# Kernel tuning notes

Hardware: AMD Instinct MI355X
Metric: run time of the kernel (lower is better)

Reference implementation:

```python
import jax, jax.numpy as jnp
import numpy as np

N, E, D_NODE, D_EDGE, F = 20000, 320000, 256, 128, 128


def _seg_mean(m, dst, w, n):
    # mean aggregation of edge messages into destination nodes
    s = jax.ops.segment_sum(m, dst, num_segments=n)
    c = jax.ops.segment_sum(w, dst, num_segments=n)
    return s / jnp.maximum(c, 1.0)[:, None]


def _edge_conv(x, e, src, dst, W, b, n, emask=None):
    # EdgeConvRot: per-edge MLP on [x_src, x_dst, edge_attr], mean-scatter to nodes
    m = jnp.concatenate([x[src], x[dst], e], axis=1) @ W + b
    if emask is not None:
        m = m * emask[:, None]
        w = emask
    else:
        w = jnp.ones((m.shape[0],), m.dtype)
    return _seg_mean(m, dst, w, n), m


def setup_inputs() -> dict:
    key = jax.random.key(0)
    ks = iter(jax.random.split(key, 40))

    def p(shape):
        return jax.random.normal(next(ks), shape, jnp.float32) / np.float32(np.sqrt(shape[0]))

    inp = {
        'node_feat': jax.random.normal(next(ks), (N, D_NODE), jnp.float32),
        'edge_feat': jax.random.normal(next(ks), (E, D_EDGE), jnp.float32),
        'edge_index': jax.random.randint(next(ks), (2, E), 0, N),
        'W_red': p((D_NODE, F)), 'b_red': jnp.zeros((F,), jnp.float32),
        'W1': p((2 * F + D_EDGE, F)), 'b1': jnp.zeros((F,), jnp.float32),
        'W2': p((3 * F, F)), 'b2': jnp.zeros((F,), jnp.float32),
        'W3': p((6 * F, F)), 'b3': jnp.zeros((F,), jnp.float32),
        'Wpre': p((3 * F, 2 * F)), 'bpre': jnp.zeros((2 * F,), jnp.float32),
        'Wsub': p((6 * F, F)), 'bsub': jnp.zeros((F,), jnp.float32),
        'W4': p((5 * F, F)), 'b4': jnp.zeros((F,), jnp.float32),
        'Wg': p((2 * F, 1)), 'a_s': p((1,)), 'a_d': p((1,)),
        'Wl1': p((F, 1)), 'bl1': jnp.zeros((1,), jnp.float32),
        'Ww': p((F, 1)), 'bw': jnp.zeros((1,), jnp.float32),
    }
    return inp


def reference(node_feat, edge_feat, edge_index, W_red, b_red, W1, b1, W2, b2,
              W3, b3, Wpre, bpre, Wsub, bsub, W4, b4, Wg, a_s, a_d,
              Wl1, bl1, Ww, bw):
    src, dst = edge_index[0], edge_index[1]
    n = node_feat.shape[0]

    x0 = node_feat @ W_red + b_red
    x1, e1 = _edge_conv(x0, edge_feat, src, dst, W1, b1, n)
    x1, e1 = jax.nn.relu(x1), jax.nn.relu(e1)
    x2, e2 = _edge_conv(x1, e1, src, dst, W2, b2, n)
    x2, e2 = jax.nn.relu(x2), jax.nn.relu(e2)
    # conv3 applied twice with SHARED weights (as in the original)
    x3, e3 = _edge_conv(jnp.concatenate([x2, x1], 1), jnp.concatenate([e2, e1], 1), src, dst, W3, b3, n)
    x3, e3 = jax.nn.relu(x3), jax.nn.relu(e3)
    x3, e3 = _edge_conv(jnp.concatenate([x3, x2], 1), jnp.concatenate([e3, e2], 1), src, dst, W3, b3, n)
    x3, e3 = jax.nn.relu(x3), jax.nn.relu(e3)

    xs1, es1 = _edge_conv(x3, e3, src, dst, Wpre, bpre, n)
    xs1, es1 = jax.nn.relu(xs1), jax.nn.relu(es1)

    # ---- SAGPooling (ratio=0.5) with single-head GATConv scorer (+self-loops) ----
    h = (xs1 @ Wg)[:, 0]                              # [N]
    loop = jnp.arange(n)
    si = jnp.concatenate([src, loop])
    di = jnp.concatenate([dst, loop])
    ea = jax.nn.leaky_relu(h[si] * a_s[0] + h[di] * a_d[0], 0.2)
    emax = jax.ops.segment_max(ea, di, num_segments=n)
    ez = jnp.exp(ea - emax[di])
    denom = jax.ops.segment_sum(ez, di, num_segments=n)
    score = jax.ops.segment_sum((ez / denom[di]) * h[si], di, num_segments=n)

    k = n // 2
    topv, perm = jax.lax.top_k(score, k)
    xp = xs1[perm] * jnp.tanh(topv)[:, None]          # [k, 2F]
    new_idx = jnp.full((n,), -1, jnp.int32).at[perm].set(jnp.arange(k, dtype=jnp.int32))
    keep = (new_idx[src] >= 0) & (new_idx[dst] >= 0)  # static-shape edge mask (filter_adj)
    sp = jnp.where(keep, new_idx[src], 0)
    dp = jnp.where(keep, new_idx[dst], 0)
    emk = keep.astype(xp.dtype)

    xs2, _ = _edge_conv(xp, es1, sp, dp, Wsub, bsub, k, emask=emk)
    xs2 = jax.nn.relu(xs2)

    # scatter merge: x3_2[perm] = x3[perm] + xs2 (perm indices are unique)
    x3_2 = x3.at[perm].add(xs2)

    x4, e4 = _edge_conv(jnp.concatenate([x3_2, x3], 1), e3, src, dst, W4, b4, n)
    x4, e4 = jax.nn.relu(x4), jax.nn.relu(e4)

    x = jax.nn.sigmoid(x4 @ Wl1 + bl1)                # [N, 1]
    w = jax.nn.sigmoid(e4 @ Ww + bw)                  # [E, 1]
    return x, w
```

## Files before the change

kernel.cpp:

```cpp
#include <hip/hip_runtime.h>
#include <cstdint>
#include <cstddef>

#define N_NODES 20000
#define N_EDGES 320000
#define EKCAP   (N_EDGES / 2)

__device__ __forceinline__ float frelu(float x){ return x > 0.f ? x : 0.f; }
__device__ __forceinline__ float fleaky(float x){ return x > 0.f ? x : 0.2f*x; }

__device__ __forceinline__ float wsum(float v){
  #pragma unroll
  for (int o = 32; o > 0; o >>= 1) v += __shfl_down(v, o);
  return v;
}
__device__ __forceinline__ float wmaxr(float v){
  #pragma unroll
  for (int o = 32; o > 0; o >>= 1) v = fmaxf(v, __shfl_down(v, o));
  return v;
}
__device__ __forceinline__ int wsumi(int v){
  #pragma unroll
  for (int o = 32; o > 0; o >>= 1) v += __shfl_down(v, o);
  return v;
}
__device__ __forceinline__ float4 fma4(float s, float4 b, float4 c){
  c.x = fmaf(s, b.x, c.x); c.y = fmaf(s, b.y, c.y);
  c.z = fmaf(s, b.z, c.z); c.w = fmaf(s, b.w, c.w); return c;
}

__global__ __launch_bounds__(256) void sgemm_k(
    const float* __restrict__ A1, int K1, const float* __restrict__ B1,
    const float* __restrict__ bias, float* __restrict__ C, int M, int Nn)
{
  __shared__ float As[16][68];
  __shared__ float Bs[16][64];
  const int t = threadIdx.x;
  const int m0 = blockIdx.y * 64, n0 = blockIdx.x * 64;
  const int tx = t & 15, ty = t >> 4;
  float acc[4][4] = {{0.f}};
  for (int kt = 0; kt < K1; kt += 16) {
    {
      const int row = t >> 2, k4 = (t & 3) * 4;
      const int gm = m0 + row;
      float4 v = make_float4(0.f, 0.f, 0.f, 0.f);
      if (gm < M) v = *(const float4*)(A1 + (size_t)gm * K1 + kt + k4);
      As[k4 + 0][row] = v.x; As[k4 + 1][row] = v.y;
      As[k4 + 2][row] = v.z; As[k4 + 3][row] = v.w;
      const int r = t >> 4, c4 = (t & 15) * 4;
      *(float4*)&Bs[r][c4] = *(const float4*)(B1 + (size_t)(kt + r) * Nn + n0 + c4);
    }
    __syncthreads();
    #pragma unroll
    for (int kk = 0; kk < 16; ++kk) {
      const float4 a = *(const float4*)&As[kk][ty * 4];
      const float4 b = *(const float4*)&Bs[kk][tx * 4];
      acc[0][0] += a.x * b.x; acc[0][1] += a.x * b.y; acc[0][2] += a.x * b.z; acc[0][3] += a.x * b.w;
      acc[1][0] += a.y * b.x; acc[1][1] += a.y * b.y; acc[1][2] += a.y * b.z; acc[1][3] += a.y * b.w;
      acc[2][0] += a.z * b.x; acc[2][1] += a.z * b.y; acc[2][2] += a.z * b.z; acc[2][3] += a.z * b.w;
      acc[3][0] += a.w * b.x; acc[3][1] += a.w * b.y; acc[3][2] += a.w * b.z; acc[3][3] += a.w * b.w;
    }
    __syncthreads();
  }
  float4 bv = make_float4(0.f, 0.f, 0.f, 0.f);
  if (bias) bv = *(const float4*)(bias + n0 + tx * 4);
  #pragma unroll
  for (int i = 0; i < 4; ++i) {
    const int gm = m0 + ty * 4 + i;
    if (gm >= M) continue;
    float4 o;
    o.x = acc[i][0] + bv.x; o.y = acc[i][1] + bv.y;
    o.z = acc[i][2] + bv.z; o.w = acc[i][3] + bv.w;
    *(float4*)(C + (size_t)gm * Nn + n0 + tx * 4) = o;
  }
}

__global__ __launch_bounds__(256) void sgemm2_k(
    const float* __restrict__ A1, int K1,
    const float* __restrict__ B1a, const float* __restrict__ B1b,
    const float* __restrict__ A2, int K2,
    const float* __restrict__ B2a, const float* __restrict__ B2b,
    const float* __restrict__ bias,
    float* __restrict__ Ca, float* __restrict__ Cb, int M, int Nn)
{
  __shared__ float As[16][68];
  __shared__ float Bs[16][64];
  const int z = blockIdx.z;
  const float* B1 = z ? B1b : B1a;
  const float* B2 = z ? B2b : B2a;
  float* C = z ? Cb : Ca;
  const float* bs = z ? nullptr : bias;
  const int t = threadIdx.x;
  const int m0 = blockIdx.y * 64, n0 = blockIdx.x * 64;
  const int tx = t & 15, ty = t >> 4;
  float acc[4][4] = {{0.f}};
  for (int pass = 0; pass < 2; ++pass) {
    const float* A = pass ? A2 : A1;
    const float* B = pass ? B2 : B1;
    const int K = pass ? K2 : K1;
    if (A == nullptr) continue;
    for (int kt = 0; kt < K; kt += 16) {
      {
        const int row = t >> 2, k4 = (t & 3) * 4;
        const int gm = m0 + row;
        float4 v = make_float4(0.f, 0.f, 0.f, 0.f);
        if (gm < M) v = *(const float4*)(A + (size_t)gm * K + kt + k4);
        As[k4 + 0][row] = v.x; As[k4 + 1][row] = v.y;
        As[k4 + 2][row] = v.z; As[k4 + 3][row] = v.w;
        const int r = t >> 4, c4 = (t & 15) * 4;
        *(float4*)&Bs[r][c4] = *(const float4*)(B + (size_t)(kt + r) * Nn + n0 + c4);
      }
      __syncthreads();
      #pragma unroll
      for (int kk = 0; kk < 16; ++kk) {
        const float4 a = *(const float4*)&As[kk][ty * 4];
        const float4 b = *(const float4*)&Bs[kk][tx * 4];
        acc[0][0] += a.x * b.x; acc[0][1] += a.x * b.y; acc[0][2] += a.x * b.z; acc[0][3] += a.x * b.w;
        acc[1][0] += a.y * b.x; acc[1][1] += a.y * b.y; acc[1][2] += a.y * b.z; acc[1][3] += a.y * b.w;
        acc[2][0] += a.z * b.x; acc[2][1] += a.z * b.y; acc[2][2] += a.z * b.z; acc[2][3] += a.z * b.w;
        acc[3][0] += a.w * b.x; acc[3][1] += a.w * b.y; acc[3][2] += a.w * b.z; acc[3][3] += a.w * b.w;
      }
      __syncthreads();
    }
  }
  float4 bv = make_float4(0.f, 0.f, 0.f, 0.f);
  if (bs) bv = *(const float4*)(bs + n0 + tx * 4);
  #pragma unroll
  for (int i = 0; i < 4; ++i) {
    const int gm = m0 + ty * 4 + i;
    if (gm >= M) continue;
    float4 o;
    o.x = acc[i][0] + bv.x; o.y = acc[i][1] + bv.y;
    o.z = acc[i][2] + bv.z; o.w = acc[i][3] + bv.w;
    *(float4*)(C + (size_t)gm * Nn + n0 + tx * 4) = o;
  }
}

#define FMA16(J) \
    acc[J][0] = fmaf(a.w, w3.x, fmaf(a.z, w2.x, fmaf(a.y, w1.x, fmaf(a.x, w0.x, acc[J][0])))); \
    acc[J][1] = fmaf(a.w, w3.y, fmaf(a.z, w2.y, fmaf(a.y, w1.y, fmaf(a.x, w0.y, acc[J][1])))); \
    acc[J][2] = fmaf(a.w, w3.z, fmaf(a.z, w2.z, fmaf(a.y, w1.z, fmaf(a.x, w0.z, acc[J][2])))); \
    acc[J][3] = fmaf(a.w, w3.w, fmaf(a.z, w2.w, fmaf(a.y, w1.w, fmaf(a.x, w0.w, acc[J][3]))));

template<int BE, int NOUT, int ASTRIDE, bool RELUIN, bool GATHER, bool STOREM, bool WHEAD, bool SUB>
__global__ __launch_bounds__(256, 4) void econv_k(
    const float* __restrict__ ein0, const float* __restrict__ ein1,
    const float* __restrict__ We,
    const float* __restrict__ P, const float* __restrict__ Q,
    const int* __restrict__ ssrc, const int* __restrict__ sdst,
    const int* __restrict__ seid, const int* __restrict__ nKp,
    float* __restrict__ mout, float* __restrict__ xsum,
    const float* __restrict__ wvec, const float* __restrict__ wb,
    float* __restrict__ outw)
{
  constexpr int NC4 = NOUT / 4;
  constexpr int TE  = 256 / NC4;
  constexpr int EPT = BE / TE;
  __shared__ float smem[8192];
  __shared__ int darr[BE], slotOf[BE], firstE[BE];
  __shared__ int dcount_s, prevd_s, nextd_s;
  const int t = threadIdx.x;
  const int base = blockIdx.x * BE;
  int nvalid = BE;
  int Elim = N_EDGES;
  if constexpr (SUB) {
    const int nK = min(*nKp, EKCAP);
    if (base >= nK) return;
    nvalid = min(BE, nK - base);
    Elim = nK;
  }
  if (t < 64) {
    if (t < BE) {
      int idx = base + t;
      if (SUB && idx >= Elim) idx = Elim - 1;
      darr[t] = sdst[idx];
    }
    if (t == 0) {
      prevd_s = (base > 0) ? sdst[base - 1] : -1;
      nextd_s = (base + BE < Elim) ? sdst[base + BE] : -1;
    }
    const int lane = t;
    const int myd = darr[(lane < BE) ? lane : (BE - 1)];
    int flag = 0;
    if (lane < BE) flag = (lane == 0) || (myd != darr[lane - 1]);
    int s = flag;
    #pragma unroll
    for (int o = 1; o < 64; o <<= 1) {
      const int v = __shfl_up(s, o);
      if (lane >= o) s += v;
    }
    if (lane < BE) {
      slotOf[lane] = s - 1;
      if (flag) firstE[s - 1] = lane;
    }
    if (lane == BE - 1) dcount_s = s;
  }
  const int tx = t % NC4, te = t / NC4;
  const int e0 = te * EPT;
  float4 acc[EPT];
  #pragma unroll
  for (int j = 0; j < EPT; ++j) acc[j] = make_float4(0.f, 0.f, 0.f, 0.f);
  const int nbuf = (ein1 != nullptr) ? 2 : 1;
  for (int buf = 0; buf < nbuf; ++buf) {
    const float* ein = buf ? ein1 : ein0;
    __syncthreads();
    #pragma unroll
    for (int i = t; i < BE * 32; i += 256) {
      const int e = i >> 5, k4 = (i & 31) * 4;
      const int g = base + e;
      const size_t row = GATHER ? (size_t)seid[g] : (size_t)g;
      float4 v = *(const float4*)(ein + row * ASTRIDE + k4);
      if (RELUIN) { v.x = frelu(v.x); v.y = frelu(v.y); v.z = frelu(v.z); v.w = frelu(v.w); }
      *(float4*)&smem[e * 128 + k4] = v;
    }
    __syncthreads();
    const float* Wb = We + (size_t)buf * 128 * NOUT + tx * 4;
    float4 wc0 = *(const float4*)(Wb + 0 * NOUT);
    float4 wc1 = *(const float4*)(Wb + 1 * NOUT);
    float4 wc2 = *(const float4*)(Wb + 2 * NOUT);
    float4 wc3 = *(const float4*)(Wb + 3 * NOUT);
    for (int kg = 0; kg < 32; ++kg) {
      const int kn = (kg < 31) ? (kg + 1) : 31;
      const float* Wn = Wb + (size_t)kn * 4 * NOUT;
      const float4 wn0 = *(const float4*)(Wn);
      const float4 wn1 = *(const float4*)(Wn + NOUT);
      const float4 wn2 = *(const float4*)(Wn + 2 * NOUT);
      const float4 wn3 = *(const float4*)(Wn + 3 * NOUT);
      #pragma unroll
      for (int j = 0; j < EPT; ++j) {
        const float4 a = *(const float4*)&smem[(e0 + j) * 128 + kg * 4];
        acc[j] = fma4(a.x, wc0, acc[j]);
        acc[j] = fma4(a.y, wc1, acc[j]);
        acc[j] = fma4(a.z, wc2, acc[j]);
        acc[j] = fma4(a.w, wc3, acc[j]);
      }
      wc0 = wn0; wc1 = wn1; wc2 = wn2; wc3 = wn3;
    }
  }
  __syncthreads();
  {
    const float4 z = make_float4(0.f, 0.f, 0.f, 0.f);
    for (int i = t * 4; i < BE * NOUT; i += 1024) *(float4*)&smem[i] = z;
  }
  __syncthreads();
  {
    float4 wv = make_float4(0.f, 0.f, 0.f, 0.f);
    if constexpr (WHEAD) wv = *(const float4*)(wvec + tx * 4);
    int cur = darr[e0];
    int slotCur = slotOf[e0];
    float4 q = *(const float4*)(Q + (size_t)cur * NOUT + tx * 4);
    float4 r = make_float4(0.f, 0.f, 0.f, 0.f);
    #pragma unroll
    for (int j = 0; j < EPT; ++j) {
      const int le = e0 + j;
      const int d = darr[le];
      if (d != cur) {
        float* a = &smem[slotCur * NOUT + tx * 4];
        atomicAdd(a + 0, r.x); atomicAdd(a + 1, r.y);
        atomicAdd(a + 2, r.z); atomicAdd(a + 3, r.w);
        cur = d; slotCur = slotOf[le];
        q = *(const float4*)(Q + (size_t)d * NOUT + tx * 4);
        r = make_float4(0.f, 0.f, 0.f, 0.f);
      }
      if (!SUB || le < nvalid) {
        const int g = base + le;
        const int s = ssrc[g];
        const float4 p = *(const float4*)(P + (size_t)s * NOUT + tx * 4);
        float4 m;
        m.x = acc[j].x + p.x + q.x; m.y = acc[j].y + p.y + q.y;
        m.z = acc[j].z + p.z + q.z; m.w = acc[j].w + p.w + q.w;
        if constexpr (STOREM) {
          *(float4*)(mout + (size_t)g * 128 + tx * 4) = m;
        }
        if constexpr (WHEAD) {
          float wp = frelu(m.x) * wv.x + frelu(m.y) * wv.y + frelu(m.z) * wv.z + frelu(m.w) * wv.w;
          #pragma unroll
          for (int o = 16; o > 0; o >>= 1) wp += __shfl_down(wp, o);
          if (tx == 0) outw[seid[g]] = 1.f / (1.f + expf(-(wp + wb[0])));
        }
        r.x += m.x; r.y += m.y; r.z += m.z; r.w += m.w;
      }
    }
    float* a = &smem[slotCur * NOUT + tx * 4];
    atomicAdd(a + 0, r.x); atomicAdd(a + 1, r.y);
    atomicAdd(a + 2, r.z); atomicAdd(a + 3, r.w);
  }
  __syncthreads();
  {
    const int dc = dcount_s;
    const int pd = prevd_s, nd = nextd_s;
    for (int i = t * 4; i < dc * NOUT; i += 1024) {
      const int sidx = i / NOUT, col = i - sidx * NOUT;
      const int d = darr[firstE[sidx]];
      const bool strad = (sidx == 0 && d == pd) || (sidx == dc - 1 && d == nd);
      const float4 v = *(const float4*)&smem[i];
      float* o = xsum + (size_t)d * NOUT + col;
      if (!strad) {
        *(float4*)o = v;
      } else {
        atomicAdd(o + 0, v.x); atomicAdd(o + 1, v.y);
        atomicAdd(o + 2, v.z); atomicAdd(o + 3, v.w);
      }
    }
  }
}

__global__ __launch_bounds__(256, 4) void presub_k(
    const float* __restrict__ e3buf, const float* __restrict__ We,
    const float* __restrict__ P, const float* __restrict__ Q,
    const int* __restrict__ csrc, const int* __restrict__ cdst,
    const int* __restrict__ cidx, const int* __restrict__ nKp,
    float* __restrict__ es1out)
{
  constexpr int BE = 32;
  const int nK = min(*nKp, EKCAP);
  const int base = blockIdx.x * BE;
  if (base >= nK) return;
  __shared__ float As[BE * 128];
  __shared__ float Ws[16 * 256];
  const int t = threadIdx.x;
  const int tx = t & 63, te = t >> 6;
  const int e0 = te * 8;
  float acc[8][4];
  #pragma unroll
  for (int j = 0; j < 8; ++j) { acc[j][0] = 0.f; acc[j][1] = 0.f; acc[j][2] = 0.f; acc[j][3] = 0.f; }
  #pragma unroll
  for (int i = t; i < BE * 32; i += 256) {
    const int e = i >> 5, k4 = (i & 31) * 4;
    const int g = base + e;
    const size_t row = (g < nK) ? (size_t)cidx[g] : 0;
    float4 v = *(const float4*)(e3buf + row * 128 + k4);
    v.x = frelu(v.x); v.y = frelu(v.y); v.z = frelu(v.z); v.w = frelu(v.w);
    *(float4*)&As[e * 128 + k4] = v;
  }
  for (int chunk = 0; chunk < 8; ++chunk) {
    __syncthreads();
    #pragma unroll
    for (int i = t; i < 16 * 64; i += 256) {
      const int r = i >> 6, c4 = (i & 63) * 4;
      *(float4*)&Ws[r * 256 + c4] = *(const float4*)(We + (size_t)(chunk * 16 + r) * 256 + c4);
    }
    __syncthreads();
    #pragma unroll
    for (int kk = 0; kk < 16; kk += 4) {
      const float4 w0 = *(const float4*)&Ws[(kk + 0) * 256 + tx * 4];
      const float4 w1 = *(const float4*)&Ws[(kk + 1) * 256 + tx * 4];
      const float4 w2 = *(const float4*)&Ws[(kk + 2) * 256 + tx * 4];
      const float4 w3 = *(const float4*)&Ws[(kk + 3) * 256 + tx * 4];
      #pragma unroll
      for (int j = 0; j < 8; ++j) {
        const float4 a = *(const float4*)&As[(e0 + j) * 128 + chunk * 16 + kk];
        FMA16(j)
      }
    }
  }
  #pragma unroll
  for (int j = 0; j < 8; ++j) {
    const int g = base + e0 + j;
    if (g < nK) {
      const int s = csrc[g], d = cdst[g];
      const float4 p = *(const float4*)(P + (size_t)s * 256 + tx * 4);
      const float4 q = *(const float4*)(Q + (size_t)d * 256 + tx * 4);
      float4 o;
      o.x = frelu(acc[j][0] + p.x + q.x); o.y = frelu(acc[j][1] + p.y + q.y);
      o.z = frelu(acc[j][2] + p.z + q.z); o.w = frelu(acc[j][3] + p.w + q.w);
      *(float4*)(es1out + (size_t)g * 256 + tx * 4) = o;
    }
  }
}

__global__ void hist_k(const int* __restrict__ dst, int* __restrict__ deg, int E){
  const int e = blockIdx.x * 256 + threadIdx.x;
  if (e < E) atomicAdd(&deg[dst[e]], 1);
}

__global__ __launch_bounds__(1024) void scan_deg_k(
    const int* __restrict__ deg, int* __restrict__ rowstart, int* __restrict__ cursor,
    float* __restrict__ recip, int n)
{
  __shared__ int sb[1024];
  __shared__ int carry;
  const int t = threadIdx.x;
  if (t == 0) carry = 0;
  __syncthreads();
  const int CH = (n + 1023) >> 10;
  for (int c = 0; c < CH; ++c) {
    const int i = c * 1024 + t;
    const int d = (i < n) ? deg[i] : 0;
    sb[t] = d;
    __syncthreads();
    for (int off = 1; off < 1024; off <<= 1) {
      const int v = (t >= off) ? sb[t - off] : 0;
      __syncthreads();
      sb[t] += v;
      __syncthreads();
    }
    const int excl = sb[t] - d;
    const int tot = sb[1023];
    if (i < n) {
      const int rs = carry + excl;
      rowstart[i] = rs; cursor[i] = rs;
      recip[i] = 1.0f / (float)max(d, 1);
    }
    __syncthreads();
    if (t == 0) carry += tot;
    __syncthreads();
  }
  if (t == 0) rowstart[n] = carry;
}

__global__ void scatter_k(const int* __restrict__ src, const int* __restrict__ dst,
                          int* __restrict__ cursor, int* __restrict__ ssrc,
                          int* __restrict__ sdst, int* __restrict__ seid, int E){
  const int e = blockIdx.x * 256 + threadIdx.x;
  if (e < E) {
    const int d = dst[e];
    const int pos = atomicAdd(&cursor[d], 1);
    ssrc[pos] = src[e]; sdst[pos] = d; seid[pos] = e;
  }
}

__global__ void meanrelu_k(const float* __restrict__ xsum, const float* __restrict__ recip,
                           float* __restrict__ out, int total, int shift){
  const int i = blockIdx.x * 256 + threadIdx.x;
  if (i < total) out[i] = frelu(xsum[i] * recip[i >> shift]);
}

__global__ void h_k(const float* __restrict__ xs1, const float* __restrict__ Wg,
                    float* __restrict__ h, int n){
  const int node = blockIdx.x * 4 + (threadIdx.x >> 6);
  const int lane = threadIdx.x & 63;
  if (node >= n) return;
  const float4 x = *(const float4*)(xs1 + (size_t)node * 256 + lane * 4);
  const float4 w = *(const float4*)(Wg + lane * 4);
  float v = x.x * w.x + x.y * w.y + x.z * w.z + x.w * w.w;
  v = wsum(v);
  if (lane == 0) h[node] = v;
}

__global__ void att_k(const float* __restrict__ h, const int* __restrict__ rowstart,
                      const int* __restrict__ ssrc, const float* __restrict__ asp,
                      const float* __restrict__ adp, float* __restrict__ score, int n){
  const int node = blockIdx.x * 4 + (threadIdx.x >> 6);
  const int lane = threadIdx.x & 63;
  if (node >= n) return;
  const float a_s = asp[0], a_d = adp[0];
  const float hv = h[node];
  const int s0 = rowstart[node], s1 = rowstart[node + 1];
  const float selfea = fleaky(hv * (a_s + a_d));
// ... 165 lines not shown
                           const int* __restrict__ cntk, const int* __restrict__ kept,
                           float* __restrict__ x32, int total){
  const int i = blockIdx.x * 256 + threadIdx.x;
  if (i >= total) return;
  const int v = i >> 7;
  float add = 0.f;
  if (kept[v]) {
    float c = (float)cntk[v];
    c = c > 0.f ? c : 1.f;
    add = frelu(xsum[i] / c);
  }
  x32[i] = x3[i] + add;
}

__global__ void fnode_k(const float* __restrict__ xsum, const float* __restrict__ recip,
                        const float* __restrict__ Wl1, const float* __restrict__ bl1,
                        float* __restrict__ out, int n){
  const int node = blockIdx.x * 4 + (threadIdx.x >> 6);
  const int lane = threadIdx.x & 63;
  if (node >= n) return;
  const float rc = recip[node];
  const float2 xv = *(const float2*)(xsum + (size_t)node * 128 + lane * 2);
  const float2 wv = *(const float2*)(Wl1 + lane * 2);
  float v = frelu(xv.x * rc) * wv.x + frelu(xv.y * rc) * wv.y;
  v = wsum(v);
  if (lane == 0) out[node] = 1.f / (1.f + expf(-(v + bl1[0])));
}

extern "C" void kernel_launch(void* const* d_in, const int* in_sizes, int n_in,
                              void* d_out, int out_size, void* d_ws, size_t ws_size,
                              hipStream_t stream)
{
  const int N = N_NODES, E = N_EDGES;
  const float* node_feat = (const float*)d_in[0];
  const float* edge_feat = (const float*)d_in[1];
  const int*   eidx      = (const int*)d_in[2];
  const float* W_red = (const float*)d_in[3];  const float* b_red = (const float*)d_in[4];
  const float* W1 = (const float*)d_in[5];   const float* b1 = (const float*)d_in[6];
  const float* W2 = (const float*)d_in[7];   const float* b2 = (const float*)d_in[8];
  const float* W3 = (const float*)d_in[9];   const float* b3 = (const float*)d_in[10];
  const float* Wpre = (const float*)d_in[11]; const float* bpre = (const float*)d_in[12];
  const float* Wsub = (const float*)d_in[13]; const float* bsub = (const float*)d_in[14];
  const float* W4 = (const float*)d_in[15];  const float* b4 = (const float*)d_in[16];
  const float* Wg = (const float*)d_in[17];
  const float* a_s = (const float*)d_in[18]; const float* a_d = (const float*)d_in[19];
  const float* Wl1 = (const float*)d_in[20]; const float* bl1 = (const float*)d_in[21];
  const float* Ww = (const float*)d_in[22];  const float* bw = (const float*)d_in[23];
  float* out_x = (float*)d_out;
  float* out_w = out_x + N;

  char* wsb = (char*)d_ws;
  size_t off = 0;
  auto alloc = [&](size_t bytes) -> void* {
    void* p = wsb + off;
    off = (off + bytes + 255) & ~(size_t)255;
    return p;
  };
  float* u1   = (float*)alloc((size_t)E * 128 * 4);
  float* u2   = (float*)alloc((size_t)E * 128 * 4);
  float* n1   = (float*)alloc((size_t)N * 128 * 4);
  float* n2   = (float*)alloc((size_t)N * 128 * 4);
  float* n3   = (float*)alloc((size_t)N * 128 * 4);
  float* xs1  = (float*)alloc((size_t)N * 256 * 4);
  float* P    = (float*)alloc((size_t)N * 256 * 4);
  float* Qb   = (float*)alloc((size_t)N * 256 * 4);
  float* xsum = (float*)alloc((size_t)N * 256 * 4);
  int* ssrc = (int*)alloc((size_t)E * 4);
  int* sdst = (int*)alloc((size_t)E * 4);
  int* seid = (int*)alloc((size_t)E * 4);
  int* csrc = (int*)alloc((size_t)E * 4);
  int* cdst = (int*)alloc((size_t)E * 4);
  int* cidx = (int*)alloc((size_t)E * 4);
  int* deg     = (int*)alloc((size_t)N * 4);
  int* cursor  = (int*)alloc((size_t)N * 4);
  int* rowstart= (int*)alloc((size_t)(N + 1) * 4);
  int* kept    = (int*)alloc((size_t)N * 4);
  int* cntk    = (int*)alloc((size_t)N * 4);
  float* recip = (float*)alloc((size_t)N * 4);
  float* hbuf  = (float*)alloc((size_t)N * 4);
  float* score = (float*)alloc((size_t)N * 4);
  float* tfac  = (float*)alloc((size_t)N * 4);
  int* bsum    = (int*)alloc(1024 * 4);
  int* Ek      = (int*)alloc(256);
  (void)ws_size; (void)in_sizes; (void)n_in; (void)out_size;

  const dim3 g128z(2, (N + 63) / 64, 2), g256z(4, (N + 63) / 64, 2);
  const dim3 g128(2, (N + 63) / 64);
  const int nbFS = (E + 1023) / 1024;
  #define NILS nullptr, nullptr, nullptr

  hipMemsetAsync(deg, 0, (size_t)N * 4, stream);
  hist_k<<<(E + 255) / 256, 256, 0, stream>>>(eidx + E, deg, E);
  scan_deg_k<<<1, 1024, 0, stream>>>(deg, rowstart, cursor, recip, N);
  scatter_k<<<(E + 255) / 256, 256, 0, stream>>>(eidx, eidx + E, cursor, ssrc, sdst, seid, E);

  sgemm_k<<<g128, 256, 0, stream>>>(node_feat, 256, W_red, b_red, n1, N, 128);

  sgemm2_k<<<g128z, 256, 0, stream>>>(n1, 128, W1, W1 + 128 * 128,
                                      nullptr, 0, nullptr, nullptr, b1, P, Qb, N, 128);
  hipMemsetAsync(xsum, 0, (size_t)N * 128 * 4, stream);
  econv_k<64, 128, 128, false, true, true, false, false><<<E / 64, 256, 0, stream>>>(
      edge_feat, nullptr, W1 + 256 * 128, P, Qb, ssrc, sdst, seid, nullptr, u1, xsum, NILS);
  meanrelu_k<<<(N * 128) / 256, 256, 0, stream>>>(xsum, recip, n2, N * 128, 7);

  sgemm2_k<<<g128z, 256, 0, stream>>>(n2, 128, W2, W2 + 128 * 128,
                                      nullptr, 0, nullptr, nullptr, b2, P, Qb, N, 128);
  hipMemsetAsync(xsum, 0, (size_t)N * 128 * 4, stream);
  econv_k<64, 128, 128, true, false, true, false, false><<<E / 64, 256, 0, stream>>>(
      u1, nullptr, W2 + 256 * 128, P, Qb, ssrc, sdst, seid, nullptr, u2, xsum, NILS);
  meanrelu_k<<<(N * 128) / 256, 256, 0, stream>>>(xsum, recip, n3, N * 128, 7);

  sgemm2_k<<<g128z, 256, 0, stream>>>(n3, 128, W3, W3 + 256 * 128,
                                      n2, 128, W3 + 128 * 128, W3 + 384 * 128, b3, P, Qb, N, 128);
  hipMemsetAsync(xsum, 0, (size_t)N * 128 * 4, stream);
  econv_k<64, 128, 128, true, false, true, false, false><<<E / 64, 256, 0, stream>>>(
      u2, u1, W3 + 512 * 128, P, Qb, ssrc, sdst, seid, nullptr, u1, xsum, NILS);
  meanrelu_k<<<(N * 128) / 256, 256, 0, stream>>>(xsum, recip, n1, N * 128, 7);

  sgemm2_k<<<g128z, 256, 0, stream>>>(n1, 128, W3, W3 + 256 * 128,
                                      n3, 128, W3 + 128 * 128, W3 + 384 * 128, b3, P, Qb, N, 128);
  hipMemsetAsync(xsum, 0, (size_t)N * 128 * 4, stream);
  econv_k<64, 128, 128, true, false, true, false, false><<<E / 64, 256, 0, stream>>>(
      u1, u2, W3 + 512 * 128, P, Qb, ssrc, sdst, seid, nullptr, u2, xsum, NILS);
  meanrelu_k<<<(N * 128) / 256, 256, 0, stream>>>(xsum, recip, n2, N * 128, 7);

  sgemm2_k<<<g256z, 256, 0, stream>>>(n2, 128, Wpre, Wpre + 128 * 256,
                                      nullptr, 0, nullptr, nullptr, bpre, P, Qb, N, 256);
  hipMemsetAsync(xsum, 0, (size_t)N * 256 * 4, stream);
  econv_k<32, 256, 128, true, false, false, false, false><<<E / 32, 256, 0, stream>>>(
      u2, nullptr, Wpre + 256 * 256, P, Qb, ssrc, sdst, seid, nullptr, nullptr, xsum, NILS);
  meanrelu_k<<<(N * 256) / 256, 256, 0, stream>>>(xsum, recip, xs1, N * 256, 8);

  h_k<<<(N + 3) / 4, 256, 0, stream>>>(xs1, Wg, hbuf, N);
  att_k<<<(N + 3) / 4, 256, 0, stream>>>(hbuf, rowstart, ssrc, a_s, a_d, score, N);
  topk_k<<<1, 1024, 0, stream>>>(score, kept, tfac, N, N / 2);
  xpip_k<<<(N * 256) / 256, 256, 0, stream>>>(xs1, tfac, N * 256);

  hipMemsetAsync(cntk, 0, (size_t)N * 4, stream);
  flagsum_k<<<nbFS, 256, 0, stream>>>(kept, ssrc, sdst, bsum, E);
  scanb_k<<<1, 512, 0, stream>>>(bsum, nbFS, Ek);
  compact_k<<<nbFS, 256, 0, stream>>>(kept, ssrc, sdst, bsum, csrc, cdst, cidx, cntk, E);

  sgemm2_k<<<g128z, 256, 0, stream>>>(xs1, 256, Wsub, Wsub + 256 * 128,
                                      nullptr, 0, nullptr, nullptr, bsub, n1, n3, N, 128);
  presub_k<<<(EKCAP + 31) / 32, 256, 0, stream>>>(
      u2, Wpre + 256 * 256, P, Qb, csrc, cdst, cidx, Ek, u1);
  hipMemsetAsync(xsum, 0, (size_t)N * 128 * 4, stream);
  econv_k<64, 128, 256, false, false, false, false, true><<<(EKCAP + 63) / 64, 256, 0, stream>>>(
      u1, u1 + 128, Wsub + 512 * 128, n1, n3, csrc, cdst, nullptr, Ek, nullptr, xsum, NILS);
  submerge_k<<<(N * 128) / 256, 256, 0, stream>>>(n2, xsum, cntk, kept, n1, N * 128);

  sgemm2_k<<<g128z, 256, 0, stream>>>(n1, 128, W4, W4 + 256 * 128,
                                      n2, 128, W4 + 128 * 128, W4 + 384 * 128, b4, P, Qb, N, 128);
  hipMemsetAsync(xsum, 0, (size_t)N * 128 * 4, stream);
  econv_k<64, 128, 128, true, false, false, true, false><<<E / 64, 256, 0, stream>>>(
      u2, nullptr, W4 + 512 * 128, P, Qb, ssrc, sdst, seid, nullptr, nullptr, xsum, Ww, bw, out_w);

  fnode_k<<<(N + 3) / 4, 256, 0, stream>>>(xsum, recip, Wl1, bl1, out_x, N);
  #undef NILS
}
```

Before: 2.592 ms.

## Run per-edge GEMMs on MFMA with split-fp16 hi/lo emulation of fp32

Replaces the scalar-FMA edge-conv kernel with an MFMA kernel. Weights and activations are split into fp16 high and low parts, and three products (hh, hl, lh) are accumulated to approximate fp32. Weights are pre-split and transposed once per call. The presub kernel is folded into the same templated kernel, and the 256-wide output layers run as two 128-wide passes. Segment aggregation now caps shared slots at 16 and falls back to global atomics. This trades extra conversion work, two launches for wide layers, and a slight precision change for much higher matrix throughput.

```diff
diff --git a/kernel.cpp b/kernel.cpp
--- a/kernel.cpp
+++ b/kernel.cpp
@@ -6,6 +6,10 @@
 #define N_EDGES 320000
 #define EKCAP   (N_EDGES / 2)
 
+typedef __attribute__((ext_vector_type(8))) _Float16 half8;
+typedef __attribute__((ext_vector_type(4))) _Float16 half4;
+typedef __attribute__((ext_vector_type(4))) float f32x4;
+
 __device__ __forceinline__ float frelu(float x){ return x > 0.f ? x : 0.f; }
 __device__ __forceinline__ float fleaky(float x){ return x > 0.f ? x : 0.2f*x; }
 
@@ -23,10 +27,6 @@
   #pragma unroll
   for (int o = 32; o > 0; o >>= 1) v += __shfl_down(v, o);
   return v;
-}
-__device__ __forceinline__ float4 fma4(float s, float4 b, float4 c){
-  c.x = fmaf(s, b.x, c.x); c.y = fmaf(s, b.y, c.y);
-  c.z = fmaf(s, b.z, c.z); c.w = fmaf(s, b.w, c.w); return c;
 }
 
 __global__ __launch_bounds__(256) void sgemm_k(
@@ -136,144 +136,208 @@
   }
 }
 
-#define FMA16(J) \
-    acc[J][0] = fmaf(a.w, w3.x, fmaf(a.z, w2.x, fmaf(a.y, w1.x, fmaf(a.x, w0.x, acc[J][0])))); \
-    acc[J][1] = fmaf(a.w, w3.y, fmaf(a.z, w2.y, fmaf(a.y, w1.y, fmaf(a.x, w0.y, acc[J][1])))); \
-    acc[J][2] = fmaf(a.w, w3.z, fmaf(a.z, w2.z, fmaf(a.y, w1.z, fmaf(a.x, w0.z, acc[J][2])))); \
-    acc[J][3] = fmaf(a.w, w3.w, fmaf(a.z, w2.w, fmaf(a.y, w1.w, fmaf(a.x, w0.w, acc[J][3]))));
-
-template<int BE, int NOUT, int ASTRIDE, bool RELUIN, bool GATHER, bool STOREM, bool WHEAD, bool SUB>
-__global__ __launch_bounds__(256, 4) void econv_k(
-    const float* __restrict__ ein0, const float* __restrict__ ein1,
-    const float* __restrict__ We,
-    const float* __restrict__ P, const float* __restrict__ Q,
+__global__ __launch_bounds__(256) void wsplit_k(
+    const float* __restrict__ We, int K, int NOUT,
+    _Float16* __restrict__ WTh, _Float16* __restrict__ WTl)
+{
+  const int id = blockIdx.x * 256 + threadIdx.x;
+  if (id >= K * NOUT) return;
+  const int k = id / NOUT, n = id - k * NOUT;
+  const float v = We[id];
+  const _Float16 h = (_Float16)v;
+  WTh[(size_t)n * K + k] = h;
+  WTl[(size_t)n * K + k] = (_Float16)(v - (float)h);
+}
+
+template<bool RELUIN, bool GATHER, bool STOREM, bool WHEAD, bool SUB, bool AGG>
+__global__ __launch_bounds__(256, 3) void econv_m(
+    const float* __restrict__ ein0, const float* __restrict__ ein1, int astride,
+    const _Float16* __restrict__ WTh, const _Float16* __restrict__ WTl,
+    const float* __restrict__ P, const float* __restrict__ Q, int pqs,
     const int* __restrict__ ssrc, const int* __restrict__ sdst,
-    const int* __restrict__ seid, const int* __restrict__ nKp,
-    float* __restrict__ mout, float* __restrict__ xsum,
+    const int* __restrict__ gidx, const int* __restrict__ seid,
+    const int* __restrict__ nKp,
+    float* __restrict__ mout, int ms,
+    float* __restrict__ xsum, int xss,
     const float* __restrict__ wvec, const float* __restrict__ wb,
     float* __restrict__ outw)
 {
-  constexpr int NC4 = NOUT / 4;
-  constexpr int TE  = 256 / NC4;
-  constexpr int EPT = BE / TE;
-  __shared__ float smem[8192];
-  __shared__ int darr[BE], slotOf[BE], firstE[BE];
+  __shared__ __align__(16) char uA[34816];
+  __shared__ __align__(16) float agg[16 * 132];
+  __shared__ int darr[64], slotOf[64], firstE[64];
   __shared__ int dcount_s, prevd_s, nextd_s;
+  _Float16* Ah = (_Float16*)uA;
+  _Float16* Al = Ah + 64 * 136;
+  float* mld = (float*)uA;
+
   const int t = threadIdx.x;
-  const int base = blockIdx.x * BE;
-  int nvalid = BE;
-  int Elim = N_EDGES;
+  const int base = blockIdx.x * 64;
+  const int nbuf = (ein1 != nullptr) ? 2 : 1;
+  int nvalid = 64, Elim = N_EDGES;
   if constexpr (SUB) {
     const int nK = min(*nKp, EKCAP);
     if (base >= nK) return;
-    nvalid = min(BE, nK - base);
+    nvalid = min(64, nK - base);
     Elim = nK;
   }
-  if (t < 64) {
-    if (t < BE) {
+  if (AGG && t < 64) {
+    {
       int idx = base + t;
       if (SUB && idx >= Elim) idx = Elim - 1;
       darr[t] = sdst[idx];
     }
     if (t == 0) {
       prevd_s = (base > 0) ? sdst[base - 1] : -1;
-      nextd_s = (base + BE < Elim) ? sdst[base + BE] : -1;
+      nextd_s = (base + 64 < Elim) ? sdst[base + 64] : -1;
     }
     const int lane = t;
-    const int myd = darr[(lane < BE) ? lane : (BE - 1)];
-    int flag = 0;
-    if (lane < BE) flag = (lane == 0) || (myd != darr[lane - 1]);
+    const int myd = darr[lane];
+    int flag = (lane == 0) || (myd != darr[lane - 1]);
     int s = flag;
     #pragma unroll
     for (int o = 1; o < 64; o <<= 1) {
       const int v = __shfl_up(s, o);
       if (lane >= o) s += v;
     }
-    if (lane < BE) {
-      slotOf[lane] = s - 1;
-      if (flag) firstE[s - 1] = lane;
-    }
-    if (lane == BE - 1) dcount_s = s;
-  }
-  const int tx = t % NC4, te = t / NC4;
-  const int e0 = te * EPT;
-  float4 acc[EPT];
-  #pragma unroll
-  for (int j = 0; j < EPT; ++j) acc[j] = make_float4(0.f, 0.f, 0.f, 0.f);
-  const int nbuf = (ein1 != nullptr) ? 2 : 1;
+    slotOf[lane] = s - 1;
+    if (flag) firstE[s - 1] = lane;
+    if (lane == 63) dcount_s = s;
+  }
+  const int lane = t & 63;
+  const int wv64 = t >> 6;
+  const int m16 = lane & 15;
+  const int q8  = (lane >> 4) * 8;
+  const int Ktot = nbuf * 128;
+  f32x4 acc[8];
+  #pragma unroll
+  for (int i = 0; i < 8; ++i) acc[i] = (f32x4)0.f;
+
   for (int buf = 0; buf < nbuf; ++buf) {
     const float* ein = buf ? ein1 : ein0;
     __syncthreads();
     #pragma unroll
-    for (int i = t; i < BE * 32; i += 256) {
-      const int e = i >> 5, k4 = (i & 31) * 4;
+    for (int i = t; i < 64 * 32; i += 256) {
+      const int e = i >> 5, kg = (i & 31) * 4;
       const int g = base + e;
-      const size_t row = GATHER ? (size_t)seid[g] : (size_t)g;
-      float4 v = *(const float4*)(ein + row * ASTRIDE + k4);
+      size_t row;
+      if (GATHER) row = (!SUB || g < Elim) ? (size_t)gidx[g] : 0;
+      else        row = (size_t)g;
+      float4 v = *(const float4*)(ein + row * astride + kg);
       if (RELUIN) { v.x = frelu(v.x); v.y = frelu(v.y); v.z = frelu(v.z); v.w = frelu(v.w); }
-      *(float4*)&smem[e * 128 + k4] = v;
-    }
-    __syncthreads();
-    const float* Wb = We + (size_t)buf * 128 * NOUT + tx * 4;
-    float4 wc0 = *(const float4*)(Wb + 0 * NOUT);
-    float4 wc1 = *(const float4*)(Wb + 1 * NOUT);
-    float4 wc2 = *(const float4*)(Wb + 2 * NOUT);
-    float4 wc3 = *(const float4*)(Wb + 3 * NOUT);
-    for (int kg = 0; kg < 32; ++kg) {
-      const int kn = (kg < 31) ? (kg + 1) : 31;
-      const float* Wn = Wb + (size_t)kn * 4 * NOUT;
-      const float4 wn0 = *(const float4*)(Wn);
-      const float4 wn1 = *(const float4*)(Wn + NOUT);
-      const float4 wn2 = *(const float4*)(Wn + 2 * NOUT);
-      const float4 wn3 = *(const float4*)(Wn + 3 * NOUT);
+      half4 hv, lv;
+      _Float16 h;
+      h = (_Float16)v.x; hv[0] = h; lv[0] = (_Float16)(v.x - (float)h);
+      h = (_Float16)v.y; hv[1] = h; lv[1] = (_Float16)(v.y - (float)h);
+      h = (_Float16)v.z; hv[2] = h; lv[2] = (_Float16)(v.z - (float)h);
+      h = (_Float16)v.w; hv[3] = h; lv[3] = (_Float16)(v.w - (float)h);
+      *(half4*)&Ah[e * 136 + kg] = hv;
+      *(half4*)&Al[e * 136 + kg] = lv;
+    }
+    __syncthreads();
+    #pragma unroll
+    for (int kk = 0; kk < 4; ++kk) {
+      const int k0 = kk * 32 + q8;
+      half8 a_h[4], a_l[4];
       #pragma unroll
-      for (int j = 0; j < EPT; ++j) {
-        const float4 a = *(const float4*)&smem[(e0 + j) * 128 + kg * 4];
-        acc[j] = fma4(a.x, wc0, acc[j]);
-        acc[j] = fma4(a.y, wc1, acc[j]);
-        acc[j] = fma4(a.z, wc2, acc[j]);
-        acc[j] = fma4(a.w, wc3, acc[j]);
+      for (int mt = 0; mt < 4; ++mt) {
+        const int m = mt * 16 + m16;
+        a_h[mt] = *(const half8*)&Ah[m * 136 + k0];
+        a_l[mt] = *(const half8*)&Al[m * 136 + k0];
       }
-      wc0 = wn0; wc1 = wn1; wc2 = wn2; wc3 = wn3;
+      #pragma unroll
+      for (int nt = 0; nt < 2; ++nt) {
+        const size_t boff = (size_t)(wv64 * 32 + nt * 16 + m16) * Ktot + buf * 128 + k0;
+        const half8 b_h = *(const half8*)(WTh + boff);
+        const half8 b_l = *(const half8*)(WTl + boff);
+        #pragma unroll
+        for (int mt = 0; mt < 4; ++mt) {
+          f32x4 c = acc[mt * 2 + nt];
+          c = __builtin_amdgcn_mfma_f32_16x16x32_f16(a_h[mt], b_h, c, 0, 0, 0);
+          c = __builtin_amdgcn_mfma_f32_16x16x32_f16(a_h[mt], b_l, c, 0, 0, 0);
+          c = __builtin_amdgcn_mfma_f32_16x16x32_f16(a_l[mt], b_h, c, 0, 0, 0);
+          acc[mt * 2 + nt] = c;
+        }
+      }
     }
   }
   __syncthreads();
   {
-    const float4 z = make_float4(0.f, 0.f, 0.f, 0.f);
-    for (int i = t * 4; i < BE * NOUT; i += 1024) *(float4*)&smem[i] = z;
+    const int qrow = (lane >> 4) * 4;
+    #pragma unroll
+    for (int mt = 0; mt < 4; ++mt) {
+      #pragma unroll
+      for (int nt = 0; nt < 2; ++nt) {
+        const int col = wv64 * 32 + nt * 16 + m16;
+        const int row = mt * 16 + qrow;
+        const f32x4 c = acc[mt * 2 + nt];
+        mld[(row + 0) * 132 + col] = c[0];
+        mld[(row + 1) * 132 + col] = c[1];
+        mld[(row + 2) * 132 + col] = c[2];
+        mld[(row + 3) * 132 + col] = c[3];
+      }
+    }
+  }
+  if constexpr (AGG) {
+    for (int i = t; i < 16 * 132; i += 256) agg[i] = 0.f;
   }
   __syncthreads();
-  {
-    float4 wv = make_float4(0.f, 0.f, 0.f, 0.f);
-    if constexpr (WHEAD) wv = *(const float4*)(wvec + tx * 4);
+  const int tx = t & 31, te = t >> 5;
+  const int e0 = te * 8;
+  if constexpr (!AGG) {
+    #pragma unroll
+    for (int j = 0; j < 8; ++j) {
+      const int le = e0 + j;
+      if (le < nvalid) {
+        const int g = base + le;
+        const int s = ssrc[g], d = sdst[g];
+        const float4 mm = *(const float4*)&mld[le * 132 + tx * 4];
+        const float4 p = *(const float4*)(P + (size_t)s * pqs + tx * 4);
+        const float4 q = *(const float4*)(Q + (size_t)d * pqs + tx * 4);
+        float4 o;
+        o.x = mm.x + p.x + q.x; o.y = mm.y + p.y + q.y;
+        o.z = mm.z + p.z + q.z; o.w = mm.w + p.w + q.w;
+        *(float4*)(mout + (size_t)g * ms + tx * 4) = o;
+      }
+    }
+    return;
+  } else {
+    float4 wvv = make_float4(0.f, 0.f, 0.f, 0.f);
+    if constexpr (WHEAD) wvv = *(const float4*)(wvec + tx * 4);
     int cur = darr[e0];
     int slotCur = slotOf[e0];
-    float4 q = *(const float4*)(Q + (size_t)cur * NOUT + tx * 4);
+    float4 q = *(const float4*)(Q + (size_t)cur * pqs + tx * 4);
     float4 r = make_float4(0.f, 0.f, 0.f, 0.f);
     #pragma unroll
-    for (int j = 0; j < EPT; ++j) {
+    for (int j = 0; j < 8; ++j) {
       const int le = e0 + j;
       const int d = darr[le];
       if (d != cur) {
-        float* a = &smem[slotCur * NOUT + tx * 4];
-        atomicAdd(a + 0, r.x); atomicAdd(a + 1, r.y);
-        atomicAdd(a + 2, r.z); atomicAdd(a + 3, r.w);
+        if (slotCur < 16) {
+          float* a = &agg[slotCur * 132 + tx * 4];
+          atomicAdd(a + 0, r.x); atomicAdd(a + 1, r.y);
+          atomicAdd(a + 2, r.z); atomicAdd(a + 3, r.w);
+        } else {
+          float* o = xsum + (size_t)cur * xss + tx * 4;
+          atomicAdd(o + 0, r.x); atomicAdd(o + 1, r.y);
+          atomicAdd(o + 2, r.z); atomicAdd(o + 3, r.w);
+        }
         cur = d; slotCur = slotOf[le];
-        q = *(const float4*)(Q + (size_t)d * NOUT + tx * 4);
+        q = *(const float4*)(Q + (size_t)d * pqs + tx * 4);
         r = make_float4(0.f, 0.f, 0.f, 0.f);
       }
       if (!SUB || le < nvalid) {
         const int g = base + le;
         const int s = ssrc[g];
-        const float4 p = *(const float4*)(P + (size_t)s * NOUT + tx * 4);
+        const float4 mm = *(const float4*)&mld[le * 132 + tx * 4];
+        const float4 p = *(const float4*)(P + (size_t)s * pqs + tx * 4);
         float4 m;
-        m.x = acc[j].x + p.x + q.x; m.y = acc[j].y + p.y + q.y;
-        m.z = acc[j].z + p.z + q.z; m.w = acc[j].w + p.w + q.w;
+        m.x = mm.x + p.x + q.x; m.y = mm.y + p.y + q.y;
+        m.z = mm.z + p.z + q.z; m.w = mm.w + p.w + q.w;
         if constexpr (STOREM) {
-          *(float4*)(mout + (size_t)g * 128 + tx * 4) = m;
+          *(float4*)(mout + (size_t)g * ms + tx * 4) = m;
         }
         if constexpr (WHEAD) {
-          float wp = frelu(m.x) * wv.x + frelu(m.y) * wv.y + frelu(m.z) * wv.z + frelu(m.w) * wv.w;
+          float wp = frelu(m.x) * wvv.x + frelu(m.y) * wvv.y + frelu(m.z) * wvv.z + frelu(m.w) * wvv.w;
           #pragma unroll
           for (int o = 16; o > 0; o >>= 1) wp += __shfl_down(wp, o);
           if (tx == 0) outw[seid[g]] = 1.f / (1.f + expf(-(wp + wb[0])));
@@ -281,90 +345,31 @@
         r.x += m.x; r.y += m.y; r.z += m.z; r.w += m.w;
       }
     }
-    float* a = &smem[slotCur * NOUT + tx * 4];
-    atomicAdd(a + 0, r.x); atomicAdd(a + 1, r.y);
-    atomicAdd(a + 2, r.z); atomicAdd(a + 3, r.w);
-  }
-  __syncthreads();
-  {
+    if (slotCur < 16) {
+      float* a = &agg[slotCur * 132 + tx * 4];
+      atomicAdd(a + 0, r.x); atomicAdd(a + 1, r.y);
+      atomicAdd(a + 2, r.z); atomicAdd(a + 3, r.w);
+    } else {
+      float* o = xsum + (size_t)cur * xss + tx * 4;
+      atomicAdd(o + 0, r.x); atomicAdd(o + 1, r.y);
+      atomicAdd(o + 2, r.z); atomicAdd(o + 3, r.w);
+    }
+    __syncthreads();
     const int dc = dcount_s;
+    const int dcl = min(dc, 16);
     const int pd = prevd_s, nd = nextd_s;
-    for (int i = t * 4; i < dc * NOUT; i += 1024) {
-      const int sidx = i / NOUT, col = i - sidx * NOUT;
-      const int d = darr[firstE[sidx]];
-      const bool strad = (sidx == 0 && d == pd) || (sidx == dc - 1 && d == nd);
-      const float4 v = *(const float4*)&smem[i];
-      float* o = xsum + (size_t)d * NOUT + col;
+    for (int i = t * 4; i < dcl * 128; i += 1024) {
+      const int slot = i >> 7, col = i & 127;
+      const int d = darr[firstE[slot]];
+      const bool strad = (slot == 0 && d == pd) || (slot == dc - 1 && d == nd);
+      const float4 v = *(const float4*)&agg[slot * 132 + col];
+      float* o = xsum + (size_t)d * xss + col;
       if (!strad) {
         *(float4*)o = v;
       } else {
         atomicAdd(o + 0, v.x); atomicAdd(o + 1, v.y);
         atomicAdd(o + 2, v.z); atomicAdd(o + 3, v.w);
       }
-    }
-  }
-}
-
-__global__ __launch_bounds__(256, 4) void presub_k(
-    const float* __restrict__ e3buf, const float* __restrict__ We,
-    const float* __restrict__ P, const float* __restrict__ Q,
-    const int* __restrict__ csrc, const int* __restrict__ cdst,
-    const int* __restrict__ cidx, const int* __restrict__ nKp,
-    float* __restrict__ es1out)
-{
-  constexpr int BE = 32;
-  const int nK = min(*nKp, EKCAP);
-  const int base = blockIdx.x * BE;
-  if (base >= nK) return;
-  __shared__ float As[BE * 128];
-  __shared__ float Ws[16 * 256];
-  const int t = threadIdx.x;
-  const int tx = t & 63, te = t >> 6;
-  const int e0 = te * 8;
-  float acc[8][4];
-  #pragma unroll
-  for (int j = 0; j < 8; ++j) { acc[j][0] = 0.f; acc[j][1] = 0.f; acc[j][2] = 0.f; acc[j][3] = 0.f; }
-  #pragma unroll
-  for (int i = t; i < BE * 32; i += 256) {
-    const int e = i >> 5, k4 = (i & 31) * 4;
-    const int g = base + e;
-    const size_t row = (g < nK) ? (size_t)cidx[g] : 0;
-    float4 v = *(const float4*)(e3buf + row * 128 + k4);
-    v.x = frelu(v.x); v.y = frelu(v.y); v.z = frelu(v.z); v.w = frelu(v.w);
-    *(float4*)&As[e * 128 + k4] = v;
-  }
-  for (int chunk = 0; chunk < 8; ++chunk) {
-    __syncthreads();
-    #pragma unroll
-    for (int i = t; i < 16 * 64; i += 256) {
-      const int r = i >> 6, c4 = (i & 63) * 4;
-      *(float4*)&Ws[r * 256 + c4] = *(const float4*)(We + (size_t)(chunk * 16 + r) * 256 + c4);
-    }
-    __syncthreads();
-    #pragma unroll
-    for (int kk = 0; kk < 16; kk += 4) {
-      const float4 w0 = *(const float4*)&Ws[(kk + 0) * 256 + tx * 4];
-      const float4 w1 = *(const float4*)&Ws[(kk + 1) * 256 + tx * 4];
-      const float4 w2 = *(const float4*)&Ws[(kk + 2) * 256 + tx * 4];
-      const float4 w3 = *(const float4*)&Ws[(kk + 3) * 256 + tx * 4];
-      #pragma unroll
-      for (int j = 0; j < 8; ++j) {
-        const float4 a = *(const float4*)&As[(e0 + j) * 128 + chunk * 16 + kk];
-        FMA16(j)
-      }
-    }
-  }
-  #pragma unroll
-  for (int j = 0; j < 8; ++j) {
-    const int g = base + e0 + j;
-    if (g < nK) {
-      const int s = csrc[g], d = cdst[g];
-      const float4 p = *(const float4*)(P + (size_t)s * 256 + tx * 4);
-      const float4 q = *(const float4*)(Q + (size_t)d * 256 + tx * 4);
-      float4 o;
-      o.x = frelu(acc[j][0] + p.x + q.x); o.y = frelu(acc[j][1] + p.y + q.y);
-      o.z = frelu(acc[j][2] + p.z + q.z); o.w = frelu(acc[j][3] + p.w + q.w);
-      *(float4*)(es1out + (size_t)g * 256 + tx * 4) = o;
     }
   }
 }
@@ -696,12 +701,26 @@
   float* tfac  = (float*)alloc((size_t)N * 4);
   int* bsum    = (int*)alloc(1024 * 4);
   int* Ek      = (int*)alloc(256);
+  _Float16* w1Th = (_Float16*)alloc(128 * 128 * 2); _Float16* w1Tl = (_Float16*)alloc(128 * 128 * 2);
+  _Float16* w2Th = (_Float16*)alloc(128 * 128 * 2); _Float16* w2Tl = (_Float16*)alloc(128 * 128 * 2);
+  _Float16* w3Th = (_Float16*)alloc(128 * 256 * 2); _Float16* w3Tl = (_Float16*)alloc(128 * 256 * 2);
+  _Float16* wpTh = (_Float16*)alloc(256 * 128 * 2); _Float16* wpTl = (_Float16*)alloc(256 * 128 * 2);
+  _Float16* wsTh = (_Float16*)alloc(128 * 256 * 2); _Float16* wsTl = (_Float16*)alloc(128 * 256 * 2);
+  _Float16* w4Th = (_Float16*)alloc(128 * 128 * 2); _Float16* w4Tl = (_Float16*)alloc(128 * 128 * 2);
   (void)ws_size; (void)in_sizes; (void)n_in; (void)out_size;
 
   const dim3 g128z(2, (N + 63) / 64, 2), g256z(4, (N + 63) / 64, 2);
   const dim3 g128(2, (N + 63) / 64);
   const int nbFS = (E + 1023) / 1024;
-  #define NILS nullptr, nullptr, nullptr
+  const int gE = E / 64, gK = (EKCAP + 63) / 64;
+  #define NIL3 nullptr, nullptr, nullptr
+
+  wsplit_k<<<(128 * 128) / 256, 256, 0, stream>>>(W1 + 256 * 128, 128, 128, w1Th, w1Tl);
+  wsplit_k<<<(128 * 128) / 256, 256, 0, stream>>>(W2 + 256 * 128, 128, 128, w2Th, w2Tl);
+  wsplit_k<<<(256 * 128) / 256, 256, 0, stream>>>(W3 + 512 * 128, 256, 128, w3Th, w3Tl);
+  wsplit_k<<<(128 * 256) / 256, 256, 0, stream>>>(Wpre + 256 * 256, 128, 256, wpTh, wpTl);
+  wsplit_k<<<(256 * 128) / 256, 256, 0, stream>>>(Wsub + 512 * 128, 256, 128, wsTh, wsTl);
+  wsplit_k<<<(128 * 128) / 256, 256, 0, stream>>>(W4 + 512 * 128, 128, 128, w4Th, w4Tl);
 
   hipMemsetAsync(deg, 0, (size_t)N * 4, stream);
   hist_k<<<(E + 255) / 256, 256, 0, stream>>>(eidx + E, deg, E);
@@ -713,36 +732,44 @@
   sgemm2_k<<<g128z, 256, 0, stream>>>(n1, 128, W1, W1 + 128 * 128,
                                       nullptr, 0, nullptr, nullptr, b1, P, Qb, N, 128);
   hipMemsetAsync(xsum, 0, (size_t)N * 128 * 4, stream);
-  econv_k<64, 128, 128, false, true, true, false, false><<<E / 64, 256, 0, stream>>>(
-      edge_feat, nullptr, W1 + 256 * 128, P, Qb, ssrc, sdst, seid, nullptr, u1, xsum, NILS);
+  econv_m<false, true, true, false, false, true><<<gE, 256, 0, stream>>>(
+      edge_feat, nullptr, 128, w1Th, w1Tl, P, Qb, 128, ssrc, sdst, seid, seid, nullptr,
+      u1, 128, xsum, 128, NIL3);
   meanrelu_k<<<(N * 128) / 256, 256, 0, stream>>>(xsum, recip, n2, N * 128, 7);
 
   sgemm2_k<<<g128z, 256, 0, stream>>>(n2, 128, W2, W2 + 128 * 128,
                                       nullptr, 0, nullptr, nullptr, b2, P, Qb, N, 128);
   hipMemsetAsync(xsum, 0, (size_t)N * 128 * 4, stream);
-  econv_k<64, 128, 128, true, false, true, false, false><<<E / 64, 256, 0, stream>>>(
-      u1, nullptr, W2 + 256 * 128, P, Qb, ssrc, sdst, seid, nullptr, u2, xsum, NILS);
+  econv_m<true, false, true, false, false, true><<<gE, 256, 0, stream>>>(
+      u1, nullptr, 128, w2Th, w2Tl, P, Qb, 128, ssrc, sdst, nullptr, nullptr, nullptr,
+      u2, 128, xsum, 128, NIL3);
   meanrelu_k<<<(N * 128) / 256, 256, 0, stream>>>(xsum, recip, n3, N * 128, 7);
 
   sgemm2_k<<<g128z, 256, 0, stream>>>(n3, 128, W3, W3 + 256 * 128,
                                       n2, 128, W3 + 128 * 128, W3 + 384 * 128, b3, P, Qb, N, 128);
   hipMemsetAsync(xsum, 0, (size_t)N * 128 * 4, stream);
-  econv_k<64, 128, 128, true, false, true, false, false><<<E / 64, 256, 0, stream>>>(
-      u2, u1, W3 + 512 * 128, P, Qb, ssrc, sdst, seid, nullptr, u1, xsum, NILS);
+  econv_m<true, false, true, false, false, true><<<gE, 256, 0, stream>>>(
+      u2, u1, 128, w3Th, w3Tl, P, Qb, 128, ssrc, sdst, nullptr, nullptr, nullptr,
+      u1, 128, xsum, 128, NIL3);
   meanrelu_k<<<(N * 128) / 256, 256, 0, stream>>>(xsum, recip, n1, N * 128, 7);
 
   sgemm2_k<<<g128z, 256, 0, stream>>>(n1, 128, W3, W3 + 256 * 128,
                                       n3, 128, W3 + 128 * 128, W3 + 384 * 128, b3, P, Qb, N, 128);
   hipMemsetAsync(xsum, 0, (size_t)N * 128 * 4, stream);
-  econv_k<64, 128, 128, true, false, true, false, false><<<E / 64, 256, 0, stream>>>(
-      u1, u2, W3 + 512 * 128, P, Qb, ssrc, sdst, seid, nullptr, u2, xsum, NILS);
+  econv_m<true, false, true, false, false, true><<<gE, 256, 0, stream>>>(
+      u1, u2, 128, w3Th, w3Tl, P, Qb, 128, ssrc, sdst, nullptr, nullptr, nullptr,
+      u2, 128, xsum, 128, NIL3);
   meanrelu_k<<<(N * 128) / 256, 256, 0, stream>>>(xsum, recip, n2, N * 128, 7);
 
   sgemm2_k<<<g256z, 256, 0, stream>>>(n2, 128, Wpre, Wpre + 128 * 256,
                                       nullptr, 0, nullptr, nullptr, bpre, P, Qb, N, 256);
   hipMemsetAsync(xsum, 0, (size_t)N * 256 * 4, stream);
-  econv_k<32, 256, 128, true, false, false, false, false><<<E / 32, 256, 0, stream>>>(
-      u2, nullptr, Wpre + 256 * 256, P, Qb, ssrc, sdst, seid, nullptr, nullptr, xsum, NILS);
+  econv_m<true, false, false, false, false, true><<<gE, 256, 0, stream>>>(
+      u2, nullptr, 128, wpTh, wpTl, P, Qb, 256, ssrc, sdst, nullptr, nullptr, nullptr,
+      nullptr, 0, xsum, 256, NIL3);
+  econv_m<true, false, false, false, false, true><<<gE, 256, 0, stream>>>(
+      u2, nullptr, 128, wpTh + 128 * 128, wpTl + 128 * 128, P + 128, Qb + 128, 256,
+      ssrc, sdst, nullptr, nullptr, nullptr, nullptr, 0, xsum + 128, 256, NIL3);
   meanrelu_k<<<(N * 256) / 256, 256, 0, stream>>>(xsum, recip, xs1, N * 256, 8);
 
   h_k<<<(N + 3) / 4, 256, 0, stream>>>(xs1, Wg, hbuf, N);
@@ -757,19 +784,25 @@
 
   sgemm2_k<<<g128z, 256, 0, stream>>>(xs1, 256, Wsub, Wsub + 256 * 128,
                                       nullptr, 0, nullptr, nullptr, bsub, n1, n3, N, 128);
-  presub_k<<<(EKCAP + 31) / 32, 256, 0, stream>>>(
-      u2, Wpre + 256 * 256, P, Qb, csrc, cdst, cidx, Ek, u1);
+  econv_m<true, true, true, false, true, false><<<gK, 256, 0, stream>>>(
+      u2, nullptr, 128, wpTh, wpTl, P, Qb, 256, csrc, cdst, cidx, nullptr, Ek,
+      u1, 256, nullptr, 0, NIL3);
+  econv_m<true, true, true, false, true, false><<<gK, 256, 0, stream>>>(
+      u2, nullptr, 128, wpTh + 128 * 128, wpTl + 128 * 128, P + 128, Qb + 128, 256,
+      csrc, cdst, cidx, nullptr, Ek, u1 + 128, 256, nullptr, 0, NIL3);
   hipMemsetAsync(xsum, 0, (size_t)N * 128 * 4, stream);
-  econv_k<64, 128, 256, false, false, false, false, true><<<(EKCAP + 63) / 64, 256, 0, stream>>>(
-      u1, u1 + 128, Wsub + 512 * 128, n1, n3, csrc, cdst, nullptr, Ek, nullptr, xsum, NILS);
+  econv_m<true, false, false, false, true, true><<<gK, 256, 0, stream>>>(
+      u1, u1 + 128, 256, wsTh, wsTl, n1, n3, 128, csrc, cdst, nullptr, nullptr, Ek,
+      nullptr, 0, xsum, 128, NIL3);
   submerge_k<<<(N * 128) / 256, 256, 0, stream>>>(n2, xsum, cntk, kept, n1, N * 128);
 
   sgemm2_k<<<g128z, 256, 0, stream>>>(n1, 128, W4, W4 + 256 * 128,
                                       n2, 128, W4 + 128 * 128, W4 + 384 * 128, b4, P, Qb, N, 128);
   hipMemsetAsync(xsum, 0, (size_t)N * 128 * 4, stream);
-  econv_k<64, 128, 128, true, false, false, true, false><<<E / 64, 256, 0, stream>>>(
-      u2, nullptr, W4 + 512 * 128, P, Qb, ssrc, sdst, seid, nullptr, nullptr, xsum, Ww, bw, out_w);
+  econv_m<true, false, false, true, false, true><<<gE, 256, 0, stream>>>(
+      u2, nullptr, 128, w4Th, w4Tl, P, Qb, 128, ssrc, sdst, nullptr, seid, nullptr,
+      nullptr, 0, xsum, 128, Ww, bw, out_w);
 
   fnode_k<<<(N + 3) / 4, 256, 0, stream>>>(xsum, recip, Wl1, bl1, out_x, N);
-  #undef NILS
-}
+  #undef NIL3
+}
```

New measurement: 2.087 ms. -19.5%, faster.
